# Kernel optimization log

Hardware: AMD Instinct MI355X
Metric: run time of the kernel (lower is better)

The kernel has to match this reference:

```python
import jax, jax.numpy as jnp
import numpy as np

BATCH = 4096
CTX = 20
HASH = 1_000_000        # word_hash_size / num_classes
DIM = 128               # word_embedding_size
NUM_SAMPLED = 8192
NEG_INF = -1e9          # accidental-hit masking (TF subtracts a huge constant)


def _log_expected_count(ids):
    # TF LogUniformCandidateSampler: P(c) = (log(c+2) - log(c+1)) / log(range_max + 1)
    # expected_count(c) = -expm1(num_sampled * log1p(-P(c)))  (sampling w/o replacement approx)
    ids_f = ids.astype(jnp.float32)
    p = (jnp.log(ids_f + 2.0) - jnp.log(ids_f + 1.0)) / jnp.log(jnp.float32(HASH + 1))
    return jnp.log(-jnp.expm1(jnp.float32(NUM_SAMPLED) * jnp.log1p(-p)))


def setup_inputs() -> dict:
    key = jax.random.key(0)
    k1, k2, k3, k4, k5, k6 = jax.random.split(key, 6)
    return {
        "input_ids": jax.random.randint(k1, (BATCH, CTX), 0, HASH, dtype=jnp.int64)
        if jax.config.jax_enable_x64 else jax.random.randint(k1, (BATCH, CTX), 0, HASH).astype(jnp.int32),
        "labels": jax.random.randint(k2, (BATCH,), 0, HASH).astype(jnp.int32),
        "sampled_ids": jax.random.randint(k3, (NUM_SAMPLED,), 0, HASH).astype(jnp.int32),
        "input_emb": jax.random.normal(k4, (HASH, DIM), dtype=jnp.float32) * 0.05,
        "output_emb": jax.random.normal(k5, (HASH, DIM), dtype=jnp.float32) * 0.05,
        "output_bias": jax.random.normal(k6, (HASH,), dtype=jnp.float32) * 0.05,
    }


def reference(input_ids, labels, sampled_ids, input_emb, output_emb, output_bias):
    # --- input-side: gather + sum-pool over context window -> [B, D]
    h = jnp.sum(input_emb[input_ids], axis=1)

    # --- sampled softmax (training path of the model) ---
    # true logits: per-example dot with the true class row  -> [B]
    w_true = output_emb[labels]                      # [B, D]
    true_logits = jnp.einsum("bd,bd->b", h, w_true) + output_bias[labels]
    true_logits = true_logits - _log_expected_count(labels)

    # sampled logits: shared negative set -> [B, S]
    w_samp = output_emb[sampled_ids]                 # [S, D]
    sampled_logits = jnp.einsum("bd,sd->bs", h, w_samp) + output_bias[sampled_ids][None, :]
    sampled_logits = sampled_logits - _log_expected_count(sampled_ids)[None, :]

    # remove accidental hits (sampled id == true label)
    hit = sampled_ids[None, :] == labels[:, None]    # [B, S]
    sampled_logits = jnp.where(hit, jnp.float32(NEG_INF), sampled_logits)

    # softmax cross entropy with the true class at column 0
    logits = jnp.concatenate([true_logits[:, None], sampled_logits], axis=1)  # [B, 1+S]
    loss = jax.nn.logsumexp(logits, axis=1) - true_logits                      # [B]
    return loss
```

## Files before the change

### kernel.cpp

```cpp
#include <hip/hip_runtime.h>
#include <hip/hip_bf16.h>
#include <math.h>

#define BATCH 4096
#define CTX 20
#define DIM 128
#define NSAMP 8192
#define NCHUNK 64

typedef __attribute__((ext_vector_type(8))) short short8;
typedef __attribute__((ext_vector_type(4))) float f32x4;

__device__ __forceinline__ unsigned short f2bf(float x) {
    union { float f; unsigned u; } v; v.f = x;
    unsigned r = v.u + 0x7FFFu + ((v.u >> 16) & 1u);
    return (unsigned short)(r >> 16);
}

__device__ __forceinline__ float eigen_plogf(float xf) {
    union { float f; unsigned u; } v; v.f = xf;
    int ei = (int)((v.u >> 23) & 0xFFu) - 126;
    v.u = (v.u & 0x007FFFFFu) | 0x3F000000u;
    float x = v.f;
    float e = (float)ei;
    bool msk = x < 0.707106781186547524f;
    float tmp = msk ? x : 0.0f;
    x = __fsub_rn(x, 1.0f);
    e = __fsub_rn(e, msk ? 1.0f : 0.0f);
    x = __fadd_rn(x, tmp);

    float x2 = __fmul_rn(x, x);
    float x3 = __fmul_rn(x2, x);

    float y, y1, y2;
    y  = __builtin_fmaf( 7.0376836292E-2f, x, -1.1514610310E-1f);
    y1 = __builtin_fmaf(-1.2420140846E-1f, x,  1.4249322787E-1f);
    y2 = __builtin_fmaf( 2.0000714765E-1f, x, -2.4999993993E-1f);
    y  = __builtin_fmaf(y,  x,  1.1676998740E-1f);
    y1 = __builtin_fmaf(y1, x, -1.6668057665E-1f);
    y2 = __builtin_fmaf(y2, x,  3.3333331174E-1f);
    y  = __builtin_fmaf(y,  x3, y1);
    y  = __builtin_fmaf(y,  x3, y2);
    y  = __fmul_rn(y, x3);

    y1  = __fmul_rn(e, -2.12194440e-4f);
    tmp = __fmul_rn(x2, 0.5f);
    y   = __fadd_rn(y, y1);
    x   = __fsub_rn(x, tmp);
    y2  = __fmul_rn(e, 0.693359375f);
    x   = __fadd_rn(x, y);
    x   = __fadd_rn(x, y2);
    return x;
}

__device__ __forceinline__ float log_expected_count(int id) {
    float idf = (float)id;
    float l2 = eigen_plogf(__fadd_rn(idf, 2.0f));
    float l1 = eigen_plogf(__fadd_rn(idf, 1.0f));
    float num = __fsub_rn(l2, l1);
    float logH = eigen_plogf(1000001.0f);
    float p = num / logH;
    float t = __fmul_rn(8192.0f, log1pf(-p));
    float e = -expm1f(t);
    e = fmaxf(e, 1e-38f);
    return logf(e);
}


__global__ void k_prep_h(const int* __restrict__ ids, const int* __restrict__ labels,
                         const float* __restrict__ in_emb, const float* __restrict__ out_emb,
                         const float* __restrict__ bias,
                         unsigned short* __restrict__ h_frag, float* __restrict__ tl) {
    int b = blockIdx.x;
    int lane = threadIdx.x;
    float ax = 0.f, ay = 0.f;
#pragma unroll
    for (int c = 0; c < CTX; ++c) {
        int id = ids[b * CTX + c];
        const float2 v = ((const float2*)(in_emb + (size_t)id * DIM))[lane];
        ax += v.x; ay += v.y;
    }
    ushort2 hb; hb.x = f2bf(ax); hb.y = f2bf(ay);
    int k0 = 2 * lane;
    int ks = k0 >> 5, kgf = (k0 >> 3) & 3, j = k0 & 7;
    size_t off = (size_t)(((b >> 4) * 4 + ks) * 512) + (kgf * 16 + (b & 15)) * 8 + j;
    *(ushort2*)(h_frag + off) = hb;

    int lab = labels[b];
    const float2 w = ((const float2*)(out_emb + (size_t)lab * DIM))[lane];
    float prod = ax * w.x + ay * w.y;
#pragma unroll
    for (int m = 32; m > 0; m >>= 1) prod += __shfl_xor(prod, m, 64);
    if (lane == 0) tl[b] = prod + bias[lab] - log_expected_count(lab);
}

__global__ void k_prep_w(const int* __restrict__ sampled, const float* __restrict__ out_emb,
                         const float* __restrict__ bias,
                         unsigned short* __restrict__ w_frag, float* __restrict__ sb) {
    int s = blockIdx.x;
    int lane = threadIdx.x;
    int sid = sampled[s];
    const float2 v = ((const float2*)(out_emb + (size_t)sid * DIM))[lane];
    ushort2 wb; wb.x = f2bf(v.x); wb.y = f2bf(v.y);
    int k0 = 2 * lane;
    int ks = k0 >> 5, kgf = (k0 >> 3) & 3, j = k0 & 7;
    size_t off = (size_t)(((s >> 4) * 4 + ks) * 512) + (kgf * 16 + (s & 15)) * 8 + j;
    *(ushort2*)(w_frag + off) = wb;
    if (lane == 0) sb[s] = bias[sid] - log_expected_count(sid);
}

__global__ __launch_bounds__(256) void k_gemm_lse(
    const unsigned short* __restrict__ h_frag, const unsigned short* __restrict__ w_frag,
    const float* __restrict__ sb, const int* __restrict__ sampled,
    const int* __restrict__ labels, float* __restrict__ partials) {
    __shared__ __align__(16) unsigned short ldsb[16384];
    int tid  = threadIdx.x;
    int lane = tid & 63;
    int wv   = tid >> 6;
    int r16  = lane & 15;
    int kg   = lane >> 4;
    int rbase = blockIdx.x * 128 + wv * 32;
    int cbase = blockIdx.y * 128;

    const unsigned short* wsrc = w_frag + (size_t)cbase * 128;
#pragma unroll
    for (int i = 0; i < 8; ++i) {
        size_t o = (size_t)(i * 256 + tid) * 8;
        *(short8*)(ldsb + o) = *(const short8*)(wsrc + o);
    }

    short8 a[2][4];
#pragma unroll
    for (int rt = 0; rt < 2; ++rt)
#pragma unroll
        for (int ks = 0; ks < 4; ++ks)
            a[rt][ks] = *(const short8*)(h_frag +
                (size_t)((((rbase >> 4) + rt) * 4 + ks) * 512) + lane * 8);

    f32x4 acc[2][8];
#pragma unroll
    for (int rt = 0; rt < 2; ++rt)
#pragma unroll
        for (int t = 0; t < 8; ++t) acc[rt][t] = (f32x4){0.f, 0.f, 0.f, 0.f};

    __syncthreads();
#pragma unroll
    for (int t = 0; t < 8; ++t) {
#pragma unroll
        for (int ks = 0; ks < 4; ++ks) {
            short8 bv = *(const short8*)(ldsb + (t * 4 + ks) * 512 + lane * 8);
            acc[0][t] = __builtin_amdgcn_mfma_f32_16x16x32_bf16(a[0][ks], bv, acc[0][t], 0, 0, 0);
            acc[1][t] = __builtin_amdgcn_mfma_f32_16x16x32_bf16(a[1][ks], bv, acc[1][t], 0, 0, 0);
        }
    }

    int lab[2][4]; int grow[2][4];
    float rsum[2][4];
#pragma unroll
    for (int rt = 0; rt < 2; ++rt)
#pragma unroll
        for (int r = 0; r < 4; ++r) {
            grow[rt][r] = rbase + rt * 16 + kg * 4 + r;
            lab[rt][r]  = labels[grow[rt][r]];
            rsum[rt][r] = 0.f;
        }
#pragma unroll
    for (int t = 0; t < 8; ++t) {
        int col = cbase + t * 16 + r16;
        float sbv = sb[col];
        int   sid = sampled[col];
#pragma unroll
        for (int rt = 0; rt < 2; ++rt)
#pragma unroll
            for (int r = 0; r < 4; ++r) {
                float logit = acc[rt][t][r] + sbv;
                if (sid != lab[rt][r]) rsum[rt][r] += __expf(logit);
            }
    }
#pragma unroll
    for (int m = 1; m < 16; m <<= 1)
#pragma unroll
        for (int rt = 0; rt < 2; ++rt)
#pragma unroll
            for (int r = 0; r < 4; ++r)
                rsum[rt][r] += __shfl_xor(rsum[rt][r], m, 64);
    if (r16 == 0)
#pragma unroll
        for (int rt = 0; rt < 2; ++rt)
#pragma unroll
            for (int r = 0; r < 4; ++r)
                partials[(size_t)grow[rt][r] * NCHUNK + blockIdx.y] = rsum[rt][r];
}

__global__ void k_reduce(const float* __restrict__ partials, const float* __restrict__ tl,
                         float* __restrict__ out) {
    int row  = blockIdx.x * 4 + (threadIdx.x >> 6);
    int lane = threadIdx.x & 63;
    float s = partials[(size_t)row * NCHUNK + lane];
#pragma unroll
    for (int m = 32; m > 0; m >>= 1) s += __shfl_xor(s, m, 64);
    if (lane == 0) {
        float t = tl[row];
        out[row] = logf(s + __expf(t)) - t;
    }
}

extern "C" void kernel_launch(void* const* d_in, const int* in_sizes, int n_in,
                              void* d_out, int out_size, void* d_ws, size_t ws_size,
                              hipStream_t stream) {
    const int*   ids     = (const int*)d_in[0];
    const int*   labels  = (const int*)d_in[1];
    const int*   sampled = (const int*)d_in[2];
    const float* in_emb  = (const float*)d_in[3];
    const float* out_emb = (const float*)d_in[4];
    const float* bias    = (const float*)d_in[5];
    float* out = (float*)d_out;

    char* ws = (char*)d_ws;
    unsigned short* h_frag = (unsigned short*)(ws);
    unsigned short* w_frag = (unsigned short*)(ws + (1u << 20));
    float* tl       = (float*)(ws + 3u * (1u << 20));
    float* sb       = (float*)(ws + 3u * (1u << 20) + (1u << 16));
    float* partials = (float*)(ws + 3u * (1u << 20) + (1u << 16) + (1u << 15));

    k_prep_h<<<dim3(BATCH), dim3(64), 0, stream>>>(ids, labels, in_emb, out_emb, bias, h_frag, tl);
    k_prep_w<<<dim3(NSAMP), dim3(64), 0, stream>>>(sampled, out_emb, bias, w_frag, sb);
    k_gemm_lse<<<dim3(BATCH / 128, NSAMP / 128), dim3(256), 0, stream>>>(h_frag, w_frag, sb, sampled, labels, partials);
    k_reduce<<<dim3(BATCH / 4), dim3(256), 0, stream>>>(partials, tl, out);
}
```

Measured before the change: 38.79 us.

## Merge prep kernels, double GEMM row tile, stage W via global_load_lds

Fuses the two gather/prep kernels into a single launch whose blocks are split by blockIdx, which removes one kernel launch and lets the two gathers run concurrently. The GEMM block now covers 256 rows (64 per wave, four row tiles), so each LDS-staged W tile is reused across twice as many rows and the grid shrinks to 16x64 blocks. The W tile is copied with direct global-to-LDS loads instead of going through registers. The cost is higher register pressure (a 4x8 grid of accumulators, with launch bounds requesting 2 blocks per unit) and fewer blocks available to hide latency.

```diff
diff --git a/kernel.cpp b/kernel.cpp
--- a/kernel.cpp
+++ b/kernel.cpp
@@ -67,49 +67,46 @@
 }
 
 
-__global__ void k_prep_h(const int* __restrict__ ids, const int* __restrict__ labels,
-                         const float* __restrict__ in_emb, const float* __restrict__ out_emb,
-                         const float* __restrict__ bias,
-                         unsigned short* __restrict__ h_frag, float* __restrict__ tl) {
-    int b = blockIdx.x;
+__global__ void k_prep(const int* __restrict__ ids, const int* __restrict__ labels,
+                       const int* __restrict__ sampled,
+                       const float* __restrict__ in_emb, const float* __restrict__ out_emb,
+                       const float* __restrict__ bias,
+                       unsigned short* __restrict__ h_frag, unsigned short* __restrict__ w_frag,
+                       float* __restrict__ tl, float* __restrict__ sb) {
     int lane = threadIdx.x;
-    float ax = 0.f, ay = 0.f;
-#pragma unroll
-    for (int c = 0; c < CTX; ++c) {
-        int id = ids[b * CTX + c];
-        const float2 v = ((const float2*)(in_emb + (size_t)id * DIM))[lane];
-        ax += v.x; ay += v.y;
-    }
-    ushort2 hb; hb.x = f2bf(ax); hb.y = f2bf(ay);
     int k0 = 2 * lane;
     int ks = k0 >> 5, kgf = (k0 >> 3) & 3, j = k0 & 7;
-    size_t off = (size_t)(((b >> 4) * 4 + ks) * 512) + (kgf * 16 + (b & 15)) * 8 + j;
-    *(ushort2*)(h_frag + off) = hb;
-
-    int lab = labels[b];
-    const float2 w = ((const float2*)(out_emb + (size_t)lab * DIM))[lane];
-    float prod = ax * w.x + ay * w.y;
-#pragma unroll
-    for (int m = 32; m > 0; m >>= 1) prod += __shfl_xor(prod, m, 64);
-    if (lane == 0) tl[b] = prod + bias[lab] - log_expected_count(lab);
-}
-
-__global__ void k_prep_w(const int* __restrict__ sampled, const float* __restrict__ out_emb,
-                         const float* __restrict__ bias,
-                         unsigned short* __restrict__ w_frag, float* __restrict__ sb) {
-    int s = blockIdx.x;
-    int lane = threadIdx.x;
-    int sid = sampled[s];
-    const float2 v = ((const float2*)(out_emb + (size_t)sid * DIM))[lane];
-    ushort2 wb; wb.x = f2bf(v.x); wb.y = f2bf(v.y);
-    int k0 = 2 * lane;
-    int ks = k0 >> 5, kgf = (k0 >> 3) & 3, j = k0 & 7;
-    size_t off = (size_t)(((s >> 4) * 4 + ks) * 512) + (kgf * 16 + (s & 15)) * 8 + j;
-    *(ushort2*)(w_frag + off) = wb;
-    if (lane == 0) sb[s] = bias[sid] - log_expected_count(sid);
-}
-
-__global__ __launch_bounds__(256) void k_gemm_lse(
+    if (blockIdx.x < BATCH) {
+        int b = blockIdx.x;
+        float ax = 0.f, ay = 0.f;
+#pragma unroll
+        for (int c = 0; c < CTX; ++c) {
+            int id = ids[b * CTX + c];
+            const float2 v = ((const float2*)(in_emb + (size_t)id * DIM))[lane];
+            ax += v.x; ay += v.y;
+        }
+        ushort2 hb; hb.x = f2bf(ax); hb.y = f2bf(ay);
+        size_t off = (size_t)(((b >> 4) * 4 + ks) * 512) + (kgf * 16 + (b & 15)) * 8 + j;
+        *(ushort2*)(h_frag + off) = hb;
+
+        int lab = labels[b];
+        const float2 w = ((const float2*)(out_emb + (size_t)lab * DIM))[lane];
+        float prod = ax * w.x + ay * w.y;
+#pragma unroll
+        for (int m = 32; m > 0; m >>= 1) prod += __shfl_xor(prod, m, 64);
+        if (lane == 0) tl[b] = prod + bias[lab] - log_expected_count(lab);
+    } else {
+        int s = blockIdx.x - BATCH;
+        int sid = sampled[s];
+        const float2 v = ((const float2*)(out_emb + (size_t)sid * DIM))[lane];
+        ushort2 wb; wb.x = f2bf(v.x); wb.y = f2bf(v.y);
+        size_t off = (size_t)(((s >> 4) * 4 + ks) * 512) + (kgf * 16 + (s & 15)) * 8 + j;
+        *(ushort2*)(w_frag + off) = wb;
+        if (lane == 0) sb[s] = bias[sid] - log_expected_count(sid);
+    }
+}
+
+__global__ __launch_bounds__(256, 2) void k_gemm_lse(
     const unsigned short* __restrict__ h_frag, const unsigned short* __restrict__ w_frag,
     const float* __restrict__ sb, const int* __restrict__ sampled,
     const int* __restrict__ labels, float* __restrict__ partials) {
@@ -119,27 +116,30 @@
     int wv   = tid >> 6;
     int r16  = lane & 15;
     int kg   = lane >> 4;
-    int rbase = blockIdx.x * 128 + wv * 32;
+    int rbase = blockIdx.x * 256 + wv * 64;
     int cbase = blockIdx.y * 128;
 
     const unsigned short* wsrc = w_frag + (size_t)cbase * 128;
 #pragma unroll
     for (int i = 0; i < 8; ++i) {
-        size_t o = (size_t)(i * 256 + tid) * 8;
-        *(short8*)(ldsb + o) = *(const short8*)(wsrc + o);
-    }
-
-    short8 a[2][4];
-#pragma unroll
-    for (int rt = 0; rt < 2; ++rt)
+        int eo = (i * 256 + tid) * 8;
+        __builtin_amdgcn_global_load_lds(
+            (const __attribute__((address_space(1))) unsigned int*)(wsrc + eo),
+            (__attribute__((address_space(3))) unsigned int*)(ldsb + eo),
+            16, 0, 0);
+    }
+
+    short8 a[4][4];
+#pragma unroll
+    for (int rt = 0; rt < 4; ++rt)
 #pragma unroll
         for (int ks = 0; ks < 4; ++ks)
             a[rt][ks] = *(const short8*)(h_frag +
                 (size_t)((((rbase >> 4) + rt) * 4 + ks) * 512) + lane * 8);
 
-    f32x4 acc[2][8];
-#pragma unroll
-    for (int rt = 0; rt < 2; ++rt)
+    f32x4 acc[4][8];
+#pragma unroll
+    for (int rt = 0; rt < 4; ++rt)
 #pragma unroll
         for (int t = 0; t < 8; ++t) acc[rt][t] = (f32x4){0.f, 0.f, 0.f, 0.f};
 
@@ -149,19 +149,19 @@
 #pragma unroll
         for (int ks = 0; ks < 4; ++ks) {
             short8 bv = *(const short8*)(ldsb + (t * 4 + ks) * 512 + lane * 8);
-            acc[0][t] = __builtin_amdgcn_mfma_f32_16x16x32_bf16(a[0][ks], bv, acc[0][t], 0, 0, 0);
-            acc[1][t] = __builtin_amdgcn_mfma_f32_16x16x32_bf16(a[1][ks], bv, acc[1][t], 0, 0, 0);
+#pragma unroll
+            for (int rt = 0; rt < 4; ++rt)
+                acc[rt][t] = __builtin_amdgcn_mfma_f32_16x16x32_bf16(a[rt][ks], bv, acc[rt][t], 0, 0, 0);
         }
     }
 
-    int lab[2][4]; int grow[2][4];
-    float rsum[2][4];
-#pragma unroll
-    for (int rt = 0; rt < 2; ++rt)
+    int lab[4][4];
+    float rsum[4][4];
+#pragma unroll
+    for (int rt = 0; rt < 4; ++rt)
 #pragma unroll
         for (int r = 0; r < 4; ++r) {
-            grow[rt][r] = rbase + rt * 16 + kg * 4 + r;
-            lab[rt][r]  = labels[grow[rt][r]];
+            lab[rt][r]  = labels[rbase + rt * 16 + kg * 4 + r];
             rsum[rt][r] = 0.f;
         }
 #pragma unroll
@@ -170,7 +170,7 @@
         float sbv = sb[col];
         int   sid = sampled[col];
 #pragma unroll
-        for (int rt = 0; rt < 2; ++rt)
+        for (int rt = 0; rt < 4; ++rt)
 #pragma unroll
             for (int r = 0; r < 4; ++r) {
                 float logit = acc[rt][t][r] + sbv;
@@ -180,16 +180,16 @@
 #pragma unroll
     for (int m = 1; m < 16; m <<= 1)
 #pragma unroll
-        for (int rt = 0; rt < 2; ++rt)
+        for (int rt = 0; rt < 4; ++rt)
 #pragma unroll
             for (int r = 0; r < 4; ++r)
                 rsum[rt][r] += __shfl_xor(rsum[rt][r], m, 64);
     if (r16 == 0)
 #pragma unroll
-        for (int rt = 0; rt < 2; ++rt)
+        for (int rt = 0; rt < 4; ++rt)
 #pragma unroll
             for (int r = 0; r < 4; ++r)
-                partials[(size_t)grow[rt][r] * NCHUNK + blockIdx.y] = rsum[rt][r];
+                partials[(size_t)(rbase + rt * 16 + kg * 4 + r) * NCHUNK + blockIdx.y] = rsum[rt][r];
 }
 
 __global__ void k_reduce(const float* __restrict__ partials, const float* __restrict__ tl,
@@ -223,8 +223,8 @@
     float* sb       = (float*)(ws + 3u * (1u << 20) + (1u << 16));
     float* partials = (float*)(ws + 3u * (1u << 20) + (1u << 16) + (1u << 15));
 
-    k_prep_h<<<dim3(BATCH), dim3(64), 0, stream>>>(ids, labels, in_emb, out_emb, bias, h_frag, tl);
-    k_prep_w<<<dim3(NSAMP), dim3(64), 0, stream>>>(sampled, out_emb, bias, w_frag, sb);
-    k_gemm_lse<<<dim3(BATCH / 128, NSAMP / 128), dim3(256), 0, stream>>>(h_frag, w_frag, sb, sampled, labels, partials);
+    k_prep<<<dim3(BATCH + NSAMP), dim3(64), 0, stream>>>(ids, labels, sampled, in_emb, out_emb, bias,
+                                                         h_frag, w_frag, tl, sb);
+    k_gemm_lse<<<dim3(BATCH / 256, NSAMP / 128), dim3(256), 0, stream>>>(h_frag, w_frag, sb, sampled, labels, partials);
     k_reduce<<<dim3(BATCH / 4), dim3(256), 0, stream>>>(partials, tl, out);
 }
```

New measurement: 36.75 us. 1.06x faster.
